# Kernel optimization log

Hardware: AMD Instinct MI355X
Metric: run time of the kernel (lower is better)

Reference implementation:

```python
import jax, jax.numpy as jnp
import numpy as np

INPUT_SIZE = 1024
HIDDEN_SIZE = 1024
B, L = 32, 2048


def setup_inputs() -> dict:
    key = jax.random.key(0)
    k_h, k_m, k_lw, k_vw, k_vq = jax.random.split(key, 5)
    h = jax.random.normal(k_h, (B, L, INPUT_SIZE), dtype=jnp.float32)
    mask = jax.random.randint(k_m, (B, L), 0, 2).astype(bool)
    # nn.Linear(input+hidden, hidden): weight (hidden, input+hidden), bias (hidden,)
    fan = INPUT_SIZE + HIDDEN_SIZE + HIDDEN_SIZE
    ln_w = jax.random.uniform(k_lw, (HIDDEN_SIZE, INPUT_SIZE + HIDDEN_SIZE),
                              minval=-1.0, maxval=1.0, dtype=jnp.float32) * np.sqrt(6.0 / fan)
    ln_b = jnp.zeros((HIDDEN_SIZE,), dtype=jnp.float32)
    # v: Linear(hidden, 1, bias=False) -> weight (1, hidden); store as (hidden,)
    v_w = jax.random.uniform(k_vw, (HIDDEN_SIZE,), minval=-1.0, maxval=1.0,
                             dtype=jnp.float32) * np.sqrt(6.0 / (HIDDEN_SIZE + 1))
    vq = jax.random.uniform(k_vq, (HIDDEN_SIZE,), dtype=jnp.float32)
    return {"h": h, "mask": mask, "ln_w": ln_w, "ln_b": ln_b, "v_w": v_w, "vq": vq}


def reference(h, mask, ln_w, ln_b, v_w, vq):
    # ln(cat([h, vq], -1)) == h @ W_h^T + vq @ W_vq^T + b  (vq is constant over b,l)
    W_h = ln_w[:, :INPUT_SIZE]          # (H, I)
    W_vq = ln_w[:, INPUT_SIZE:]         # (H, H)
    bias = ln_b + W_vq @ vq             # (H,)
    pre = jnp.einsum('bli,hi->blh', h, W_h) + bias  # (B, L, H)
    s = jnp.tanh(pre) @ v_w             # (B, L)
    s = s - (~mask).astype(s.dtype) * 10000.0
    a = jax.nn.softmax(s, axis=1)       # softmax over seq dim
    r = jnp.einsum('bl,bli->bi', a, h)  # (B, I)
    return r  # dropout omitted (eval mode)
```

## Files before the change

kernel.cpp:

```cpp
#include <hip/hip_runtime.h>
#include <hip/hip_bf16.h>

typedef short  bf16x8s __attribute__((ext_vector_type(8)));
typedef float  f32x4   __attribute__((ext_vector_type(4)));

#define BATCH 32
#define SEQL  2048
#define NROWS (BATCH * SEQL)
#define IN    1024
#define HID   1024

#define WHB_OFF   0u
#define BIAS_OFF  0x200000u
#define SPART_OFF 0x210000u
#define ABUF_OFF  0x610000u
#define HB_OFF    0x650000u
#define WS_NEED_BF16 ((size_t)HB_OFF + (size_t)NROWS * IN * 2)

__device__ __forceinline__ unsigned int pack2bf(float f0, float f1) {
    unsigned int u0 = __float_as_uint(f0) + 0x8000u;
    unsigned int u1 = __float_as_uint(f1) + 0x8000u;
    return __builtin_amdgcn_perm(u1, u0, 0x07060302u);
}

__device__ __forceinline__ float tanh_fast(float x) {
    float xc = fminf(fmaxf(x, -15.f), 15.f);
    float t  = __builtin_amdgcn_exp2f(xc * 2.8853900817779268f);
    return (t - 1.f) * __builtin_amdgcn_rcpf(t + 1.f);
}

__device__ __forceinline__ void gl2lds16(const void* g, void* l) {
    __builtin_amdgcn_global_load_lds(
        (const __attribute__((address_space(1))) unsigned int*)g,
        (__attribute__((address_space(3))) unsigned int*)l, 16, 0, 0);
}

__device__ __forceinline__ void block_map(int bi, int& rb, int& cb) {
    int xcd  = bi & 7;
    int slot = bi >> 3;
    rb = xcd + 8 * (slot >> 3);
    cb = slot & 7;
}

__global__ __launch_bounds__(256) void prep_kernel(const float* __restrict__ ln_w,
                                                   const float* __restrict__ ln_b,
                                                   const float* __restrict__ vq,
                                                   const float* __restrict__ h,
                                                   unsigned short* __restrict__ whb,
                                                   float* __restrict__ bias,
                                                   unsigned short* __restrict__ hb) {
    const int bi = blockIdx.x;
    const int t  = threadIdx.x;
    if (bi < 1024) {
        const int n = bi;
        const int wave = t >> 6;
        const int lane = t & 63;
        float4 v = ((const float4*)(ln_w + (size_t)n * 2048))[t];
        uint2 pk;
        pk.x = pack2bf(v.x, v.y);
        pk.y = pack2bf(v.z, v.w);
        *(uint2*)(whb + (size_t)n * 1024 + t * 4) = pk;
        const float* wrow = ln_w + (size_t)n * 2048 + 1024;
        float s = 0.f;
        #pragma unroll
        for (int j = 0; j < 4; ++j) {
            int k = t + j * 256;
            s += wrow[k] * vq[k];
        }
        #pragma unroll
        for (int off = 32; off; off >>= 1) s += __shfl_xor(s, off);
        __shared__ float red[4];
        if (lane == 0) red[wave] = s;
        __syncthreads();
        if (t == 0) bias[n] = ln_b[n] + red[0] + red[1] + red[2] + red[3];
    } else {
        size_t idx = ((size_t)(bi - 1024) * 256 + t) * 8;
        float4 a = *(const float4*)(h + idx);
        float4 b = *(const float4*)(h + idx + 4);
        uint4 p;
        p.x = pack2bf(a.x, a.y); p.y = pack2bf(a.z, a.w);
        p.z = pack2bf(b.x, b.y); p.w = pack2bf(b.z, b.w);
        *(uint4*)(hb + idx) = p;
    }
}

__global__ __launch_bounds__(512) void gemm256_kernel(const unsigned short* __restrict__ hb,
                                                      const unsigned short* __restrict__ whb,
                                                      const float* __restrict__ bias,
                                                      const float* __restrict__ vw,
                                                      float* __restrict__ s_part) {
    __shared__ __align__(16) unsigned short As[2][8192];
    __shared__ __align__(16) unsigned short Bs[2][4096];

    const int tid = threadIdx.x;
    int rb, cb;
    block_map(blockIdx.x, rb, cb);
    const int wave = tid >> 6;
    const int lane = tid & 63;
    const int quad = lane >> 4;
    const int l15  = lane & 15;
    const int wy   = wave >> 1;
    const int wx   = wave & 1;
    const int row0 = rb * 256;
    const int col0 = cb * 128;

    const int srow = tid >> 2;
    const int sg   = tid & 3;
    const int swz  = (srow >> 1) & 3;
    const unsigned short* gA0 = hb  + (size_t)(row0 + srow) * 1024 + ((sg ^ swz) * 8);
    const unsigned short* gA1 = gA0 + (size_t)128 * 1024;
    const unsigned short* gB0 = whb + (size_t)(col0 + srow) * 1024 + ((sg ^ swz) * 8);
    const int dA0 = tid * 8;
    const int dA1 = 4096 + tid * 8;
    const int dB0 = tid * 8;

    const unsigned short* rA[4];
    const unsigned short* rB[4];
    #pragma unroll
    for (int i = 0; i < 4; ++i) {
        int ra = wy * 64 + i * 16 + l15;
        rA[i] = &As[0][0] + ra * 32 + ((quad ^ ((ra >> 1) & 3)) * 8);
        int rn = wx * 64 + i * 16 + l15;
        rB[i] = &Bs[0][0] + rn * 32 + ((quad ^ ((rn >> 1) & 3)) * 8);
    }

    f32x4 acc[4][4];
    #pragma unroll
    for (int i = 0; i < 4; ++i)
        #pragma unroll
        for (int j = 0; j < 4; ++j)
            acc[i][j] = (f32x4){0.f, 0.f, 0.f, 0.f};

    gl2lds16(gA0, &As[0][dA0]);
    gl2lds16(gA1, &As[0][dA1]);
    gl2lds16(gB0, &Bs[0][dB0]);
    __syncthreads();

    int cur = 0;
    for (int k0 = 0; k0 < 1024; k0 += 32) {
        if (k0 + 32 < 1024) {
            const int nxt = cur ^ 1;
            gl2lds16(gA0 + k0 + 32, &As[nxt][dA0]);
            gl2lds16(gA1 + k0 + 32, &As[nxt][dA1]);
            gl2lds16(gB0 + k0 + 32, &Bs[nxt][dB0]);
        }

        const int aoff = cur * 8192;
        const int boff = cur * 4096;
        bf16x8s af[4], bfv[4];
        #pragma unroll
        for (int i = 0; i < 4; ++i) af[i]  = *(const bf16x8s*)(rA[i] + aoff);
        #pragma unroll
        for (int i = 0; i < 4; ++i) bfv[i] = *(const bf16x8s*)(rB[i] + boff);
        #pragma unroll
        for (int mt = 0; mt < 4; ++mt)
            #pragma unroll
            for (int nt = 0; nt < 4; ++nt)
                acc[mt][nt] = __builtin_amdgcn_mfma_f32_16x16x32_bf16(af[mt], bfv[nt], acc[mt][nt], 0, 0, 0);

        __syncthreads();
        cur ^= 1;
    }

    const int colb = col0 + wx * 64 + l15;
    float vwv[4], bv[4];
    #pragma unroll
    for (int nt = 0; nt < 4; ++nt) {
        vwv[nt] = vw[colb + nt * 16];
        bv[nt]  = bias[colb + nt * 16];
    }
    const int rowb = row0 + wy * 64 + quad * 4;
    const int colp = cb * 2 + wx;
    #pragma unroll
    for (int mt = 0; mt < 4; ++mt) {
        #pragma unroll
        for (int r = 0; r < 4; ++r) {
            float p = 0.f;
            #pragma unroll
            for (int nt = 0; nt < 4; ++nt)
                p += tanh_fast(acc[mt][nt][r] + bv[nt]) * vwv[nt];
            p += __shfl_xor(p, 1);
            p += __shfl_xor(p, 2);
            p += __shfl_xor(p, 4);
            p += __shfl_xor(p, 8);
            if (l15 == 0) s_part[(size_t)(rowb + mt * 16 + r) * 16 + colp] = p;
        }
    }
}

__global__ __launch_bounds__(256) void gemm_f32_kernel(const float* __restrict__ hmat,
                                                       const unsigned short* __restrict__ whb,
                                                       const float* __restrict__ bias,
                                                       const float* __restrict__ vw,
                                                       float* __restrict__ s_part) {
    __shared__ __align__(16) unsigned short As[4096];
    __shared__ __align__(16) unsigned short Bs[4096];
    const int tid = threadIdx.x;
    int rb, cb;
    block_map(blockIdx.x, rb, cb);
    const int wave = tid >> 6;
    const int lane = tid & 63;
    const int quad = lane >> 4;
    const int l15  = lane & 15;
    const int wy   = wave >> 1;
    const int wx   = wave & 1;
    const int row0 = rb * 128;
    const int col0 = cb * 128;
    const int srow = tid >> 2;
    const int sg   = tid & 3;
    const int swz  = (srow >> 1) & 3;
    const float*          gA0 = hmat + (size_t)(row0 + srow)      * 1024 + sg * 8;
    const float*          gA1 = hmat + (size_t)(row0 + srow + 64) * 1024 + sg * 8;
    const unsigned short* gB0 = whb  + (size_t)(col0 + srow)      * 1024 + ((sg ^ swz) * 8);
    unsigned short* wA0 = As + srow * 32 + ((sg ^ swz) * 8);
    unsigned short* wA1 = wA0 + 64 * 32;
    unsigned short* lB0 = Bs + tid * 8;
    const unsigned short* rA[4];
    const unsigned short* rB[4];
    #pragma unroll
    for (int i = 0; i < 4; ++i) {
        int ra = wy * 64 + i * 16 + l15;
        rA[i] = As + ra * 32 + ((quad ^ ((ra >> 1) & 3)) * 8);
        int rn = wx * 64 + i * 16 + l15;
        rB[i] = Bs + rn * 32 + ((quad ^ ((rn >> 1) & 3)) * 8);
    }
    f32x4 acc[4][4];
    #pragma unroll
    for (int i = 0; i < 4; ++i)
        #pragma unroll
        for (int j = 0; j < 4; ++j)
            acc[i][j] = (f32x4){0.f, 0.f, 0.f, 0.f};
    for (int k0 = 0; k0 < 1024; k0 += 32) {
        float4 va0 = *(const float4*)(gA0 + k0);
        float4 va1 = *(const float4*)(gA0 + k0 + 4);
        float4 va2 = *(const float4*)(gA1 + k0);
        float4 va3 = *(const float4*)(gA1 + k0 + 4);
        __syncthreads();
        gl2lds16(gB0 + k0, lB0);
        gl2lds16(gB0 + 65536 + k0, lB0 + 2048);
        uint4 pa0, pa1;
        pa0.x = pack2bf(va0.x, va0.y); pa0.y = pack2bf(va0.z, va0.w);
        pa0.z = pack2bf(va1.x, va1.y); pa0.w = pack2bf(va1.z, va1.w);
        pa1.x = pack2bf(va2.x, va2.y); pa1.y = pack2bf(va2.z, va2.w);
        pa1.z = pack2bf(va3.x, va3.y); pa1.w = pack2bf(va3.z, va3.w);
        *(uint4*)wA0 = pa0;
        *(uint4*)wA1 = pa1;
        __syncthreads();
        bf16x8s af[4], bfv[4];
        #pragma unroll
        for (int i = 0; i < 4; ++i) af[i]  = *(const bf16x8s*)rA[i];
        #pragma unroll
        for (int i = 0; i < 4; ++i) bfv[i] = *(const bf16x8s*)rB[i];
        #pragma unroll
        for (int mt = 0; mt < 4; ++mt)
            #pragma unroll
            for (int nt = 0; nt < 4; ++nt)
                acc[mt][nt] = __builtin_amdgcn_mfma_f32_16x16x32_bf16(af[mt], bfv[nt], acc[mt][nt], 0, 0, 0);
    }
    const int colb = col0 + wx * 64 + l15;
    float vwv[4], bv[4];
    #pragma unroll
    for (int nt = 0; nt < 4; ++nt) {
        vwv[nt] = vw[colb + nt * 16];
        bv[nt]  = bias[colb + nt * 16];
    }
    const int rowb = row0 + wy * 64 + quad * 4;
    const int colp = cb * 2 + wx;
    #pragma unroll
    for (int mt = 0; mt < 4; ++mt) {
        #pragma unroll
        for (int r = 0; r < 4; ++r) {
            float p = 0.f;
            #pragma unroll
            for (int nt = 0; nt < 4; ++nt)
                p += tanh_fast(acc[mt][nt][r] + bv[nt]) * vwv[nt];
            p += __shfl_xor(p, 1);
            p += __shfl_xor(p, 2);
            p += __shfl_xor(p, 4);
            p += __shfl_xor(p, 8);
            if (l15 == 0) s_part[(size_t)(rowb + mt * 16 + r) * 16 + colp] = p;
        }
    }
}

__global__ __launch_bounds__(512) void softmax_kernel(const float* __restrict__ s_part,
                                                      const int* __restrict__ mask,
                                                      float* __restrict__ a_buf,
                                                      float* __restrict__ out) {
    const int b    = blockIdx.x;
    const int t    = threadIdx.x;
    const int wave = t >> 6;
    const int lane = t & 63;
    ((float2*)(out + b * 1024))[t] = (float2){0.f, 0.f};
    __shared__ float redm[8];
    __shared__ float reds[8];
    float sv[4];
    float mx = -3.0e38f;
    #pragma unroll
    for (int j = 0; j < 4; ++j) {
        int l = t + j * 512;
        const float4* pr = (const float4*)(s_part + ((size_t)b * 2048 + l) * 16);
        float4 q0 = pr[0], q1 = pr[1], q2 = pr[2], q3 = pr[3];
        float v = (q0.x + q0.y + q0.z + q0.w) + (q1.x + q1.y + q1.z + q1.w)
                + (q2.x + q2.y + q2.z + q2.w) + (q3.x + q3.y + q3.z + q3.w);
        if (mask[b * 2048 + l] == 0) v -= 10000.f;
        sv[j] = v;
        mx = fmaxf(mx, v);
    }
    #pragma unroll
    for (int off = 32; off; off >>= 1) mx = fmaxf(mx, __shfl_xor(mx, off));
    if (lane == 0) redm[wave] = mx;
    __syncthreads();
    mx = redm[0];
    #pragma unroll
    for (int w = 1; w < 8; ++w) mx = fmaxf(mx, redm[w]);
    float sum = 0.f;
    #pragma unroll
    for (int j = 0; j < 4; ++j) {
        sv[j] = __expf(sv[j] - mx);
        sum += sv[j];
    }
    #pragma unroll
    for (int off = 32; off; off >>= 1) sum += __shfl_xor(sum, off);
    if (lane == 0) reds[wave] = sum;
    __syncthreads();
    sum = reds[0];
    #pragma unroll
    for (int w = 1; w < 8; ++w) sum += reds[w];
    float inv = 1.f / sum;
    #pragma unroll
    for (int j = 0; j < 4; ++j)
        a_buf[b * 2048 + t + j * 512] = sv[j] * inv;
}

__global__ __launch_bounds__(256) void r_bf16_kernel(const unsigned short* __restrict__ hb,
                                                     const float* __restrict__ a_buf,
                                                     float* __restrict__ out) {
    const int b  = blockIdx.x >> 5;
    const int lc = blockIdx.x & 31;
    const int t  = threadIdx.x;
    __shared__ float aw[64];
    if (t < 64) aw[t] = a_buf[b * 2048 + lc * 64 + t];
    __syncthreads();
    const uint2* hp = (const uint2*)(hb + (size_t)(b * 2048 + lc * 64) * 1024) + t;
    float a0 = 0.f, a1 = 0.f, a2 = 0.f, a3 = 0.f;
    #pragma unroll 8
    for (int l = 0; l < 64; ++l) {
        uint2 v = hp[(size_t)l * 256];
        float av = aw[l];
        a0 += av * __uint_as_float(v.x << 16);
        a1 += av * __uint_as_float(v.x & 0xffff0000u);
        a2 += av * __uint_as_float(v.y << 16);
        a3 += av * __uint_as_float(v.y & 0xffff0000u);
    }
    float* op = out + b * 1024 + t * 4;
    atomicAdd(op + 0, a0);
    atomicAdd(op + 1, a1);
    atomicAdd(op + 2, a2);
    atomicAdd(op + 3, a3);
}

__global__ __launch_bounds__(256) void r_f32_kernel(const float* __restrict__ hmat,
                                                    const float* __restrict__ a_buf,
                                                    float* __restrict__ out) {
    const int b  = blockIdx.x >> 5;
    const int lc = blockIdx.x & 31;
    const int t  = threadIdx.x;
    __shared__ float aw[64];
    if (t < 64) aw[t] = a_buf[b * 2048 + lc * 64 + t];
    __syncthreads();
    const float4* hp = (const float4*)hmat + (size_t)(b * 2048 + lc * 64) * 256;
    float ax = 0.f, ay = 0.f, az = 0.f, aq = 0.f;
    #pragma unroll 8
    for (int l = 0; l < 64; ++l) {
        float4 hv = hp[(size_t)l * 256 + t];
        float av = aw[l];
        ax += av * hv.x; ay += av * hv.y; az += av * hv.z; aq += av * hv.w;
    }
    float* op = out + b * 1024 + t * 4;
    atomicAdd(op + 0, ax);
    atomicAdd(op + 1, ay);
    atomicAdd(op + 2, az);
    atomicAdd(op + 3, aq);
}

extern "C" void kernel_launch(void* const* d_in, const int* in_sizes, int n_in,
                              void* d_out, int out_size, void* d_ws, size_t ws_size,
                              hipStream_t stream) {
    const float* h    = (const float*)d_in[0];
    const int*   mask = (const int*)d_in[1];
    const float* ln_w = (const float*)d_in[2];
    const float* ln_b = (const float*)d_in[3];
    const float* v_w  = (const float*)d_in[4];
    const float* vq   = (const float*)d_in[5];
    float* out = (float*)d_out;

    char* ws = (char*)d_ws;
    unsigned short* whb = (unsigned short*)(ws + WHB_OFF);
    float* bias         = (float*)(ws + BIAS_OFF);
    float* s_part       = (float*)(ws + SPART_OFF);
    float* a_buf        = (float*)(ws + ABUF_OFF);
    unsigned short* hb  = (unsigned short*)(ws + HB_OFF);

    const bool use_bf16_h = (ws_size >= WS_NEED_BF16);

    if (use_bf16_h) {
        prep_kernel<<<1024 + 32768, 256, 0, stream>>>(ln_w, ln_b, vq, h, whb, bias, hb);
        gemm256_kernel<<<(NROWS / 256) * (HID / 128), 512, 0, stream>>>(hb, whb, bias, v_w, s_part);
        softmax_kernel<<<BATCH, 512, 0, stream>>>(s_part, mask, a_buf, out);
        r_bf16_kernel<<<BATCH * 32, 256, 0, stream>>>(hb, a_buf, out);
    } else {
        prep_kernel<<<1024, 256, 0, stream>>>(ln_w, ln_b, vq, h, whb, bias, hb);
        gemm_f32_kernel<<<(NROWS / 128) * (HID / 128), 256, 0, stream>>>(h, whb, bias, v_w, s_part);
        softmax_kernel<<<BATCH, 512, 0, stream>>>(s_part, mask, a_buf, out);
        r_f32_kernel<<<BATCH * 32, 256, 0, stream>>>(h, a_buf, out);
    }
}
```

Baseline: 643.2 us.

## Single-buffer GEMM LDS tiles and replace atomic output reduction with partial buffers

The bf16 GEMM drops its double-buffered LDS prefetch and instead loads each K-slice, synchronises, then computes, which halves LDS use and may allow more resident blocks, but it removes the overlap between global loads and MFMA. Separately, the weighted-sum kernels no longer zero the output and atomically add into it. They write per-chunk partials to a workspace buffer that reuses the score region, and a new reduce kernel sums them. This gives a deterministic reduction without atomics at the cost of an extra launch and extra memory traffic.

```diff
diff --git a/kernel.cpp b/kernel.cpp
--- a/kernel.cpp
+++ b/kernel.cpp
@@ -15,6 +15,7 @@
 #define SPART_OFF 0x210000u
 #define ABUF_OFF  0x610000u
 #define HB_OFF    0x650000u
+#define RPART_OFF SPART_OFF
 #define WS_NEED_BF16 ((size_t)HB_OFF + (size_t)NROWS * IN * 2)
 
 __device__ __forceinline__ unsigned int pack2bf(float f0, float f1) {
@@ -89,8 +90,8 @@
                                                       const float* __restrict__ bias,
                                                       const float* __restrict__ vw,
                                                       float* __restrict__ s_part) {
-    __shared__ __align__(16) unsigned short As[2][8192];
-    __shared__ __align__(16) unsigned short Bs[2][4096];
+    __shared__ __align__(16) unsigned short As[8192];
+    __shared__ __align__(16) unsigned short Bs[4096];
 
     const int tid = threadIdx.x;
     int rb, cb;
@@ -110,18 +111,18 @@
     const unsigned short* gA0 = hb  + (size_t)(row0 + srow) * 1024 + ((sg ^ swz) * 8);
     const unsigned short* gA1 = gA0 + (size_t)128 * 1024;
     const unsigned short* gB0 = whb + (size_t)(col0 + srow) * 1024 + ((sg ^ swz) * 8);
-    const int dA0 = tid * 8;
-    const int dA1 = 4096 + tid * 8;
-    const int dB0 = tid * 8;
+    unsigned short* lA0 = As + tid * 8;
+    unsigned short* lA1 = As + 4096 + tid * 8;
+    unsigned short* lB0 = Bs + tid * 8;
 
     const unsigned short* rA[4];
     const unsigned short* rB[4];
     #pragma unroll
     for (int i = 0; i < 4; ++i) {
         int ra = wy * 64 + i * 16 + l15;
-        rA[i] = &As[0][0] + ra * 32 + ((quad ^ ((ra >> 1) & 3)) * 8);
+        rA[i] = As + ra * 32 + ((quad ^ ((ra >> 1) & 3)) * 8);
         int rn = wx * 64 + i * 16 + l15;
-        rB[i] = &Bs[0][0] + rn * 32 + ((quad ^ ((rn >> 1) & 3)) * 8);
+        rB[i] = Bs + rn * 32 + ((quad ^ ((rn >> 1) & 3)) * 8);
     }
 
     f32x4 acc[4][4];
@@ -131,35 +132,23 @@
         for (int j = 0; j < 4; ++j)
             acc[i][j] = (f32x4){0.f, 0.f, 0.f, 0.f};
 
-    gl2lds16(gA0, &As[0][dA0]);
-    gl2lds16(gA1, &As[0][dA1]);
-    gl2lds16(gB0, &Bs[0][dB0]);
-    __syncthreads();
-
-    int cur = 0;
     for (int k0 = 0; k0 < 1024; k0 += 32) {
-        if (k0 + 32 < 1024) {
-            const int nxt = cur ^ 1;
-            gl2lds16(gA0 + k0 + 32, &As[nxt][dA0]);
-            gl2lds16(gA1 + k0 + 32, &As[nxt][dA1]);
-            gl2lds16(gB0 + k0 + 32, &Bs[nxt][dB0]);
-        }
-
-        const int aoff = cur * 8192;
-        const int boff = cur * 4096;
+        __syncthreads();
+        gl2lds16(gA0 + k0, lA0);
+        gl2lds16(gA1 + k0, lA1);
+        gl2lds16(gB0 + k0, lB0);
+        __syncthreads();
+
         bf16x8s af[4], bfv[4];
         #pragma unroll
-        for (int i = 0; i < 4; ++i) af[i]  = *(const bf16x8s*)(rA[i] + aoff);
-        #pragma unroll
-        for (int i = 0; i < 4; ++i) bfv[i] = *(const bf16x8s*)(rB[i] + boff);
+        for (int i = 0; i < 4; ++i) af[i]  = *(const bf16x8s*)rA[i];
+        #pragma unroll
+        for (int i = 0; i < 4; ++i) bfv[i] = *(const bf16x8s*)rB[i];
         #pragma unroll
         for (int mt = 0; mt < 4; ++mt)
             #pragma unroll
             for (int nt = 0; nt < 4; ++nt)
                 acc[mt][nt] = __builtin_amdgcn_mfma_f32_16x16x32_bf16(af[mt], bfv[nt], acc[mt][nt], 0, 0, 0);
-
-        __syncthreads();
-        cur ^= 1;
     }
 
     const int colb = col0 + wx * 64 + l15;
@@ -285,13 +274,11 @@
 
 __global__ __launch_bounds__(512) void softmax_kernel(const float* __restrict__ s_part,
                                                       const int* __restrict__ mask,
-                                                      float* __restrict__ a_buf,
-                                                      float* __restrict__ out) {
+                                                      float* __restrict__ a_buf) {
     const int b    = blockIdx.x;
     const int t    = threadIdx.x;
     const int wave = t >> 6;
     const int lane = t & 63;
-    ((float2*)(out + b * 1024))[t] = (float2){0.f, 0.f};
     __shared__ float redm[8];
     __shared__ float reds[8];
     float sv[4];
@@ -333,9 +320,9 @@
         a_buf[b * 2048 + t + j * 512] = sv[j] * inv;
 }
 
-__global__ __launch_bounds__(256) void r_bf16_kernel(const unsigned short* __restrict__ hb,
-                                                     const float* __restrict__ a_buf,
-                                                     float* __restrict__ out) {
+__global__ __launch_bounds__(256) void r_bf16_part_kernel(const unsigned short* __restrict__ hb,
+                                                          const float* __restrict__ a_buf,
+                                                          float* __restrict__ r_part) {
     const int b  = blockIdx.x >> 5;
     const int lc = blockIdx.x & 31;
     const int t  = threadIdx.x;
@@ -353,16 +340,13 @@
         a2 += av * __uint_as_float(v.y << 16);
         a3 += av * __uint_as_float(v.y & 0xffff0000u);
     }
-    float* op = out + b * 1024 + t * 4;
-    atomicAdd(op + 0, a0);
-    atomicAdd(op + 1, a1);
-    atomicAdd(op + 2, a2);
-    atomicAdd(op + 3, a3);
-}
-
-__global__ __launch_bounds__(256) void r_f32_kernel(const float* __restrict__ hmat,
-                                                    const float* __restrict__ a_buf,
-                                                    float* __restrict__ out) {
+    float4 res = {a0, a1, a2, a3};
+    *(float4*)(r_part + ((size_t)lc * 32 + b) * 1024 + t * 4) = res;
+}
+
+__global__ __launch_bounds__(256) void r_f32_part_kernel(const float* __restrict__ hmat,
+                                                         const float* __restrict__ a_buf,
+                                                         float* __restrict__ r_part) {
     const int b  = blockIdx.x >> 5;
     const int lc = blockIdx.x & 31;
     const int t  = threadIdx.x;
@@ -377,11 +361,21 @@
         float av = aw[l];
         ax += av * hv.x; ay += av * hv.y; az += av * hv.z; aq += av * hv.w;
     }
-    float* op = out + b * 1024 + t * 4;
-    atomicAdd(op + 0, ax);
-    atomicAdd(op + 1, ay);
-    atomicAdd(op + 2, az);
-    atomicAdd(op + 3, aq);
+    float4 res = {ax, ay, az, aq};
+    *(float4*)(r_part + ((size_t)lc * 32 + b) * 1024 + t * 4) = res;
+}
+
+__global__ __launch_bounds__(256) void r_reduce_kernel(const float* __restrict__ r_part,
+                                                       float* __restrict__ out) {
+    const int b = blockIdx.x;
+    const int t = threadIdx.x;
+    float4 s = {0.f, 0.f, 0.f, 0.f};
+    #pragma unroll 8
+    for (int lc = 0; lc < 32; ++lc) {
+        float4 v = *(const float4*)(r_part + ((size_t)lc * 32 + b) * 1024 + t * 4);
+        s.x += v.x; s.y += v.y; s.z += v.z; s.w += v.w;
+    }
+    *(float4*)(out + b * 1024 + t * 4) = s;
 }
 
 extern "C" void kernel_launch(void* const* d_in, const int* in_sizes, int n_in,
@@ -401,18 +395,21 @@
     float* s_part       = (float*)(ws + SPART_OFF);
     float* a_buf        = (float*)(ws + ABUF_OFF);
     unsigned short* hb  = (unsigned short*)(ws + HB_OFF);
+    float* r_part       = (float*)(ws + RPART_OFF);
 
     const bool use_bf16_h = (ws_size >= WS_NEED_BF16);
 
     if (use_bf16_h) {
         prep_kernel<<<1024 + 32768, 256, 0, stream>>>(ln_w, ln_b, vq, h, whb, bias, hb);
         gemm256_kernel<<<(NROWS / 256) * (HID / 128), 512, 0, stream>>>(hb, whb, bias, v_w, s_part);
-        softmax_kernel<<<BATCH, 512, 0, stream>>>(s_part, mask, a_buf, out);
-        r_bf16_kernel<<<BATCH * 32, 256, 0, stream>>>(hb, a_buf, out);
+        softmax_kernel<<<BATCH, 512, 0, stream>>>(s_part, mask, a_buf);
+        r_bf16_part_kernel<<<BATCH * 32, 256, 0, stream>>>(hb, a_buf, r_part);
+        r_reduce_kernel<<<BATCH, 256, 0, stream>>>(r_part, out);
     } else {
         prep_kernel<<<1024, 256, 0, stream>>>(ln_w, ln_b, vq, h, whb, bias, hb);
         gemm_f32_kernel<<<(NROWS / 128) * (HID / 128), 256, 0, stream>>>(h, whb, bias, v_w, s_part);
-        softmax_kernel<<<BATCH, 512, 0, stream>>>(s_part, mask, a_buf, out);
-        r_f32_kernel<<<BATCH * 32, 256, 0, stream>>>(h, a_buf, out);
-    }
-}
+        softmax_kernel<<<BATCH, 512, 0, stream>>>(s_part, mask, a_buf);
+        r_f32_part_kernel<<<BATCH * 32, 256, 0, stream>>>(h, a_buf, r_part);
+        r_reduce_kernel<<<BATCH, 256, 0, stream>>>(r_part, out);
+    }
+}
```

Result: faster. 554.4 us (-13.8%).
